# Optimization experiments

Hardware: AMD Instinct MI355X
Metric: run time of the kernel (lower is better)

The kernel has to match this reference:

```python
import jax, jax.numpy as jnp
import numpy as np

B, S, D = 2, 2048, 1024
H, DH = 16, 64
BS = 512            # block_size
MAX_LEN = 2048      # rope base = max_seq_length
NB = S // BS        # number of blocks (no padding: S % BS == 0)


def setup_inputs() -> dict:
    key = jax.random.key(0)
    ks = jax.random.split(key, 5)
    s = 1.0 / np.sqrt(D)
    x = jax.random.normal(ks[0], (B, S, D), jnp.float32)
    Wq = jax.random.normal(ks[1], (D, D), jnp.float32) * s
    Wk = jax.random.normal(ks[2], (D, D), jnp.float32) * s
    Wv = jax.random.normal(ks[3], (D, D), jnp.float32) * s
    Wo = jax.random.normal(ks[4], (D, D), jnp.float32) * s
    z = jnp.zeros((D,), jnp.float32)
    return {"x": x, "Wq": Wq, "bq": z, "Wk": Wk, "bk": z,
            "Wv": Wv, "bv": z, "Wo": Wo, "bo": z}


def _apply_rope(q, k):
    # inv_freq uses max_seq_length as the base (as in the source module)
    inv_freq = 1.0 / MAX_LEN ** (jnp.arange(0, DH, 2, dtype=jnp.float32) / DH)  # [DH/2]
    pos = jnp.arange(S, dtype=jnp.float32)
    freqs = jnp.outer(pos, inv_freq)                 # [S, DH/2]
    cos = jnp.cos(freqs)[None, :, None, :]           # [1,S,1,DH/2]
    sin = jnp.sin(freqs)[None, :, None, :]
    half = DH // 2
    q1, q2 = q[..., :half], q[..., half:]
    k1, k2 = k[..., :half], k[..., half:]
    q_rot = jnp.concatenate([q1 * cos - q2 * sin, q1 * sin + q2 * cos], axis=-1)
    k_rot = jnp.concatenate([k1 * cos - k2 * sin, k1 * sin + k2 * cos], axis=-1)
    return q_rot, k_rot


def _block_attn(qb, q_start, kb, vb, k_start):
    # qb,kb,vb: [B,H,BS,DH]; returns attended [B,H,BS,DH], lse [B,H,BS]
    scale = 1.0 / jnp.sqrt(DH)
    scores = jnp.einsum('bhqd,bhkd->bhqk', qb, kb) * scale
    q_pos = jnp.arange(BS) + q_start
    k_pos = jnp.arange(BS) + k_start
    mask = (q_pos[:, None] >= k_pos[None, :])[None, None]   # [1,1,BS,BS]
    scores = jnp.where(mask, scores, -1e9)
    mx = jnp.max(scores, axis=-1, keepdims=True)
    mx = jnp.where(jnp.isinf(mx), 0.0, mx)
    e = jnp.where(mask, jnp.exp(scores - mx), 0.0)
    se = jnp.sum(e, axis=-1, keepdims=True) + 1e-10
    attended = jnp.einsum('bhqk,bhkd->bhqd', e / se, vb)
    lse = (jnp.log(se) + mx)[..., 0]                        # [B,H,BS]
    return attended, lse


def _forward(x, Wq, bq, Wk, bk, Wv, bv, Wo, bo):
    q = (x @ Wq + bq).reshape(B, S, H, DH)
    k = (x @ Wk + bk).reshape(B, S, H, DH)
    v = (x @ Wv + bv).reshape(B, S, H, DH)
    q, k = _apply_rope(q, k)
    # split into blocks: [NB, B, H, BS, DH]
    def to_blocks(t):
        return t.reshape(B, NB, BS, H, DH).transpose(1, 0, 3, 2, 4)
    qb, kb, vb = to_blocks(q), to_blocks(k), to_blocks(v)
    starts = jnp.arange(NB) * BS
    inner = jax.vmap(_block_attn, in_axes=(None, None, 0, 0, 0))   # over k blocks
    outer = jax.vmap(inner, in_axes=(0, 0, None, None, None))      # over q blocks
    att, lse = outer(qb, starts, kb, vb, starts)
    # att: [NBq,NBk,B,H,BS,DH], lse: [NBq,NBk,B,H,BS]
    mlse = jnp.max(lse, axis=1, keepdims=True)
    w = jnp.exp(lse - mlse)
    w = w / (jnp.sum(w, axis=1, keepdims=True) + 1e-10)
    acc = jnp.sum(att * w[..., None], axis=1)                      # [NBq,B,H,BS,DH]
    out = acc.transpose(1, 0, 3, 2, 4).reshape(B, S, D)
    out = out @ Wo + bo
    return out


def reference(x, Wq, bq, Wk, bk, Wv, bv, Wo, bo):
    out = _forward(x, Wq, bq, Wk, bk, Wv, bv, Wo, bo)
    attention_weights = jnp.ones((B, H, S, S), jnp.float32)  # dummy, as in source
    return out, attention_weights
```

## Files before the change

kernel.cpp:

```cpp
#include <hip/hip_runtime.h>
#include <cstdint>
#include <cstddef>

#define DEVINL __device__ __forceinline__

typedef float   f32x4  __attribute__((ext_vector_type(4)));
typedef float   vf4    __attribute__((ext_vector_type(4)));
typedef __bf16  bf16x8 __attribute__((ext_vector_type(8)));
typedef uint32_t u32;
typedef unsigned short u16;
typedef uint32_t u32x4 __attribute__((ext_vector_type(4)));

constexpr int Bb = 2, Ss = 2048, Dd = 1024, Hh = 16;
constexpr int Mm = Bb * Ss;


DEVINL u16 f2bf(float f) {
  union { float f; u32 u; } a; a.f = f;
  u32 r = a.u + 0x7fffu + ((a.u >> 16) & 1u);
  return (u16)(r >> 16);
}

typedef const __attribute__((address_space(1))) void* gas_t;
typedef __attribute__((address_space(3))) void* las_t;
DEVINL void gld_lds16(const void* g, void* l) {
  __builtin_amdgcn_global_load_lds((gas_t)g, (las_t)l, 16, 0, 0);
}

__global__ void fill_ones(vf4* __restrict__ p, long long n4) {
  size_t i = (size_t)blockIdx.x * blockDim.x + threadIdx.x;
  size_t stride = (size_t)gridDim.x * blockDim.x;
  const vf4 one = {1.f, 1.f, 1.f, 1.f};
  for (; i < (size_t)n4; i += stride)
    __builtin_nontemporal_store(one, p + i);
}

__global__ void rope_table(float* __restrict__ cosT, float* __restrict__ sinT) {
  int idx = blockIdx.x * 256 + threadIdx.x;
  int s = idx >> 5, j = idx & 31;
  float freq = (float)s * exp2f(-11.0f * (float)j / 32.0f);
  cosT[idx] = cosf(freq);
  sinT[idx] = sinf(freq);
}

__global__ void cast_x(const float* __restrict__ x, u16* __restrict__ xb) {
  size_t i = ((size_t)blockIdx.x * 256 + threadIdx.x) * 4;
  vf4 v = *(const vf4*)(x + i);
  union { u16 u[4]; unsigned long long q; } o;
  o.u[0] = f2bf(v.x); o.u[1] = f2bf(v.y); o.u[2] = f2bf(v.z); o.u[3] = f2bf(v.w);
  *(unsigned long long*)(xb + i) = o.q;
}

__global__ void transpose_cast_W(const float* __restrict__ W0, const float* __restrict__ W1,
                                 const float* __restrict__ W2, const float* __restrict__ W3,
                                 u16* __restrict__ Wt) {
  __shared__ u16 tile[64][72];
  const int z = blockIdx.z;
  const float* W = (z == 0) ? W0 : (z == 1) ? W1 : (z == 2) ? W2 : W3;
  u16* Out = Wt + (size_t)z * (Dd * Dd);
  const int k0 = blockIdx.x * 64, n0 = blockIdx.y * 64;
  const int tid = threadIdx.x;
#pragma unroll
  for (int it = 0; it < 4; ++it) {
    int r = it * 16 + (tid >> 4);
    int c = (tid & 15) * 4;
    vf4 v = *(const vf4*)(W + (size_t)(k0 + r) * Dd + n0 + c);
    tile[r][c + 0] = f2bf(v.x); tile[r][c + 1] = f2bf(v.y);
    tile[r][c + 2] = f2bf(v.z); tile[r][c + 3] = f2bf(v.w);
  }
  __syncthreads();
#pragma unroll
  for (int it = 0; it < 2; ++it) {
    int c = it * 256 + tid;
    int n = c >> 3, ck = c & 7;
    union { u16 u[8]; u32x4 q; } o;
#pragma unroll
    for (int j = 0; j < 8; ++j) o.u[j] = tile[ck * 8 + j][n];
    *(u32x4*)(Out + (size_t)(n0 + n) * Dd + k0 + ck * 8) = o.q;
  }
}

DEVINL void gemm_mainloop(const u16* __restrict__ A, const u16* __restrict__ Bt,
                          int m0, int n0, char* lds, f32x4 (&acc)[4][4],
                          vf4* __restrict__ onesp, size_t obase) {
  const int tid = threadIdx.x, lane = tid & 63;
  const int w = tid >> 6, wr = w >> 1, wc = w & 1;
  const int l15 = lane & 15, l4 = lane >> 4;
  auto stage = [&](const u16* g, int row0, int k0, char* dst) {
#pragma unroll
    for (int h2 = 0; h2 < 2; ++h2) {
      int c = h2 * 256 + tid;
      const char* src = (const char*)g + (size_t)(row0 + (c >> 2)) * 2048 + k0 * 2 + (c & 3) * 16;
      gld_lds16(src, dst + c * 16);
    }
  };
  stage(A, m0, 0, lds);
  stage(Bt, n0, 0, lds + 16384);
  asm volatile("s_waitcnt vmcnt(0)");
  __syncthreads();
  const vf4 onev = {1.f, 1.f, 1.f, 1.f};
#pragma unroll 2
  for (int t = 0; t < 32; ++t) {
    const int cur = t & 1;
    char* As = lds + cur * 8192;
    char* Bs = lds + 16384 + cur * 8192;
    if (t < 31) {
      char* An = lds + (cur ^ 1) * 8192;
      char* Bn = lds + 16384 + (cur ^ 1) * 8192;
      stage(A, m0, (t + 1) * 32, An);
      stage(Bt, n0, (t + 1) * 32, Bn);
    }
    __builtin_nontemporal_store(onev, onesp + obase + (size_t)t * 256 + tid);
    bf16x8 af[4], bfr[4];
#pragma unroll
    for (int mt = 0; mt < 4; ++mt)
      af[mt] = *(const bf16x8*)(As + (wr * 64 + mt * 16 + l15) * 64 + l4 * 16);
#pragma unroll
    for (int nt = 0; nt < 4; ++nt)
      bfr[nt] = *(const bf16x8*)(Bs + (wc * 64 + nt * 16 + l15) * 64 + l4 * 16);
#pragma unroll
    for (int mt = 0; mt < 4; ++mt)
#pragma unroll
      for (int nt = 0; nt < 4; ++nt)
        acc[mt][nt] = __builtin_amdgcn_mfma_f32_16x16x32_bf16(af[mt], bfr[nt], acc[mt][nt], 0, 0, 0);
    asm volatile("s_waitcnt vmcnt(0)");
    __syncthreads();
  }
}

template <int EPI>
__global__ __launch_bounds__(256) void gemm128(
    const u16* __restrict__ A, const u16* __restrict__ W0,
    const float* __restrict__ b0, const float* __restrict__ b1, const float* __restrict__ b2,
    const float* __restrict__ cosT, const float* __restrict__ sinT,
    u16* __restrict__ Qo, u16* __restrict__ Ko, u16* __restrict__ Vo,
    float* __restrict__ outp, vf4* __restrict__ onesp) {
  __shared__ __align__(16) char lds[32768];
  const int tid = threadIdx.x, lane = tid & 63;
  const int w = tid >> 6, wr = w >> 1, wc = w & 1;
  const int l15 = lane & 15, l4 = lane >> 4;

  const int lin = blockIdx.y * 32 + blockIdx.x;
  const int xcd = lin & 7, ix = lin >> 3;
  constexpr int YPX = (EPI == 0) ? 3 : 1;
  const int ytile = xcd * YPX + (ix >> 5);
  const int m0 = (ix & 31) * 128;

  int mat, n0;
  const u16* Bt;
  if (EPI == 0) { mat = ytile >> 3; n0 = (ytile & 7) * 128; Bt = W0 + (size_t)mat * (Dd * Dd); }
  else          { mat = 0;          n0 = ytile * 128;       Bt = W0; }
  const size_t obase = (EPI == 0 ? 0 : (size_t)6291456) + (size_t)lin * 8192;

  f32x4 acc[4][4] = {};
  gemm_mainloop(A, Bt, m0, n0, lds, acc, onesp, obase);

  if (EPI == 0) {
    const float* bias = (mat == 0) ? b0 : ((mat == 1) ? b1 : b2);
    u16* Out = (mat == 0) ? Qo : ((mat == 1) ? Ko : Vo);
    const bool dorope = (mat < 2);
#pragma unroll
    for (int mt = 0; mt < 4; ++mt) {
#pragma unroll
      for (int i = 0; i < 4; ++i) {
        int m = m0 + wr * 64 + mt * 16 + l4 * 4 + i;
        int bidx = m >> 11, s = m & 2047;
        float cv0 = 0.f, sv0 = 0.f, cv1 = 0.f, sv1 = 0.f;
        if (dorope) {
          cv0 = cosT[s * 32 + l15];      sv0 = sinT[s * 32 + l15];
          cv1 = cosT[s * 32 + 16 + l15]; sv1 = sinT[s * 32 + 16 + l15];
        }
#pragma unroll
        for (int nt = 0; nt < 4; ++nt) {
          int n = n0 + wc * 64 + nt * 16 + l15;
          float v = acc[mt][nt][i] + bias[n];
          float ov;
          if (dorope) {
            int np = n0 + wc * 64 + (nt ^ 2) * 16 + l15;
            float vp = acc[mt][nt ^ 2][i] + bias[np];
            float cc = (nt & 1) ? cv1 : cv0, sn = (nt & 1) ? sv1 : sv0;
            ov = (nt < 2) ? (v * cc - vp * sn)
                          : (vp * sn + v * cc);
          } else ov = v;
          int hh = n >> 6, dh = n & 63;
          Out[(((size_t)bidx * Hh + hh) * Ss + s) * 64 + dh] = f2bf(ov);
        }
      }
    }
  } else {
#pragma unroll
    for (int mt = 0; mt < 4; ++mt)
#pragma unroll
      for (int i = 0; i < 4; ++i) {
        int m = m0 + wr * 64 + mt * 16 + l4 * 4 + i;
#pragma unroll
        for (int nt = 0; nt < 4; ++nt) {
          int n = n0 + wc * 64 + nt * 16 + l15;
          outp[(size_t)m * Dd + n] = acc[mt][nt][i] + b0[n];
        }
      }
  }
}

__global__ void transpose_v(const u16* __restrict__ Vg, u16* __restrict__ Vtg) {
  __shared__ u16 tile[64][72];
  const int s0 = blockIdx.x * 64, bh = blockIdx.y;
  const int tid = threadIdx.x;
  const u16* Vb = Vg + (size_t)bh * Ss * 64;
  u16* Vtb = Vtg + (size_t)bh * 64 * Ss;
#pragma unroll
  for (int h2 = 0; h2 < 2; ++h2) {
    int c = h2 * 256 + tid;
    int r = c >> 3, ck = c & 7;
    u32x4 v = *(const u32x4*)(Vb + (size_t)(s0 + r) * 64 + ck * 8);
    const u16* t8 = (const u16*)&v;
#pragma unroll
    for (int j = 0; j < 8; ++j) tile[r][ck * 8 + j] = t8[j];
  }
  __syncthreads();
#pragma unroll
  for (int h2 = 0; h2 < 2; ++h2) {
    int c = h2 * 256 + tid;
    int dh = c >> 3, ck = c & 7;
    union { u16 u[8]; u32x4 q; } o;
#pragma unroll
    for (int j = 0; j < 8; ++j) o.u[j] = tile[ck * 8 + j][dh];
    *(u32x4*)(Vtb + (size_t)dh * Ss + s0 + ck * 8) = o.q;
  }
}

__global__ __launch_bounds__(256) void attn_kernel(
    const u16* __restrict__ Qg, const u16* __restrict__ Kg,
    const u16* __restrict__ Vtg, u16* __restrict__ Og) {
  __shared__ __align__(16) char lds[49152];

  const int tid = threadIdx.x, lane = tid & 63, w = tid >> 6;
  const int l15 = lane & 15, l4 = lane >> 4;

  const int bid = blockIdx.x;
  const int bh = bid & 31;
  const int qt_raw = (bid >> 5) & 7;
  const int qtile = (bid >> 8) ? qt_raw : (15 - qt_raw);
  const int q0 = qtile * 128;
  const int qw = q0 + w * 32;
  const int ntiles = 2 * qtile + 2;
  const int tdiag = qw >> 6;

  const u16*  Qb  = Qg + (size_t)bh * Ss * 64;
  const char* Kb  = (const char*)(Kg + (size_t)bh * Ss * 64);
  const char* Vtb = (const char*)(Vtg + (size_t)bh * 64 * Ss);

  bf16x8 aq[2][2];
#pragma unroll
  for (int mt = 0; mt < 2; ++mt)
#pragma unroll
    for (int kt = 0; kt < 2; ++kt)
      aq[mt][kt] = *(const bf16x8*)(Qb + (size_t)(qw + mt * 16 + l15) * 64 + kt * 32 + l4 * 8);

  f32x4 accO[2][4] = {};
  float mrow[2][4], lrow[2][4];
#pragma unroll
  for (int mt = 0; mt < 2; ++mt)
#pragma unroll
    for (int i = 0; i < 4; ++i) { mrow[mt][i] = -1e30f; lrow[mt][i] = 0.f; }

  char* pw = lds + 32768 + w * 4096;

  auto stageKV = [&](int t, char* bK, char* bV) {
    const int kv0 = t * 64;
#pragma unroll
    for (int h2 = 0; h2 < 2; ++h2) {
      int c = h2 * 256 + tid;
      int r = c >> 3, ck = c & 7;
      gld_lds16(Kb + (size_t)(kv0 + r) * 128 + ((ck ^ (r & 7)) * 16), bK + c * 16);
      gld_lds16(Vtb + (size_t)r * (Ss * 2) + (size_t)kv0 * 2 + ((ck ^ (r & 7)) * 16), bV + c * 16);
    }
  };

  stageKV(0, lds, lds + 8192);
  asm volatile("s_waitcnt vmcnt(0)");
  __syncthreads();

  for (int t = 0; t < ntiles; ++t) {
    const int cur = t & 1;
    char* curb = lds + cur * 16384;
    char* nxtb = lds + (cur ^ 1) * 16384;
    if (t + 1 < ntiles) stageKV(t + 1, nxtb, nxtb + 8192);
    if (t <= tdiag) {
      const int kv0 = t * 64;
      char* ldsK = curb;
      char* ldsV = curb + 8192;

      f32x4 sf[2][4] = {};
#pragma unroll
      for (int kt = 0; kt < 2; ++kt) {
        bf16x8 bk[4];
#pragma unroll
        for (int nt = 0; nt < 4; ++nt) {
          int row = nt * 16 + l15;
          int ch = (kt * 4 + l4) ^ (row & 7);
          bk[nt] = *(const bf16x8*)(ldsK + row * 128 + ch * 16);
        }
#pragma unroll
        for (int mt = 0; mt < 2; ++mt)
#pragma unroll
          for (int nt = 0; nt < 4; ++nt)
            sf[mt][nt] = __builtin_amdgcn_mfma_f32_16x16x32_bf16(aq[mt][kt], bk[nt], sf[mt][nt], 0, 0, 0);
      }

      const bool diag = (t == tdiag);
#pragma unroll
      for (int mt = 0; mt < 2; ++mt) {
#pragma unroll
        for (int i = 0; i < 4; ++i) {
          int row = qw + mt * 16 + l4 * 4 + i;
          float sv[4];
          float mx = -1e30f;
#pragma unroll
          for (int nt = 0; nt < 4; ++nt) {
            float xv = sf[mt][nt][i] * 0.125f;
            if (diag && (kv0 + nt * 16 + l15) > row) xv = -1e30f;
            sv[nt] = xv; mx = fmaxf(mx, xv);
          }
          mx = fmaxf(mx, __shfl_xor(mx, 1));
          mx = fmaxf(mx, __shfl_xor(mx, 2));
          mx = fmaxf(mx, __shfl_xor(mx, 4));
          mx = fmaxf(mx, __shfl_xor(mx, 8));
          float mnew = fmaxf(mrow[mt][i], mx);
          float rescale = __expf(mrow[mt][i] - mnew);
          float rs = 0.f;
          int rl = mt * 16 + l4 * 4 + i;
#pragma unroll
          for (int nt = 0; nt < 4; ++nt) {
            float p = __expf(sv[nt] - mnew);
            rs += p;
            int key = nt * 16 + l15;
            int boff = rl * 128 + (((key >> 3) ^ (rl & 7)) << 4) + (key & 7) * 2;
            *(u16*)(pw + boff) = f2bf(p);
          }
          rs += __shfl_xor(rs, 1); rs += __shfl_xor(rs, 2);
          rs += __shfl_xor(rs, 4); rs += __shfl_xor(rs, 8);
          lrow[mt][i] = lrow[mt][i] * rescale + rs;
          mrow[mt][i] = mnew;
#pragma unroll
          for (int nt = 0; nt < 4; ++nt) accO[mt][nt][i] *= rescale;
        }
      }

#pragma unroll
      for (int ks = 0; ks < 2; ++ks) {
        bf16x8 ap[2], bv[4];
#pragma unroll
        for (int mt = 0; mt < 2; ++mt) {
          int row = mt * 16 + l15;
          int ch = (ks * 4 + l4) ^ (row & 7);
          ap[mt] = *(const bf16x8*)(pw + row * 128 + ch * 16);
        }
#pragma unroll
        for (int nt = 0; nt < 4; ++nt) {
          int row = nt * 16 + l15;
          int ch = (ks * 4 + l4) ^ (row & 7);
          bv[nt] = *(const bf16x8*)(ldsV + row * 128 + ch * 16);
        }
#pragma unroll
        for (int mt = 0; mt < 2; ++mt)
#pragma unroll
          for (int nt = 0; nt < 4; ++nt)
            accO[mt][nt] = __builtin_amdgcn_mfma_f32_16x16x32_bf16(ap[mt], bv[nt], accO[mt][nt], 0, 0, 0);
      }
    }
    asm volatile("s_waitcnt vmcnt(0)");
    __syncthreads();
  }

  const int b = bh >> 4, h = bh & 15;
#pragma unroll
  for (int mt = 0; mt < 2; ++mt)
#pragma unroll
    for (int i = 0; i < 4; ++i) {
      int s = qw + mt * 16 + l4 * 4 + i;
      float inv = 1.0f / (lrow[mt][i] + 1e-10f);
      size_t rowbase = ((size_t)b * Ss + s) * Dd + h * 64;
#pragma unroll
      for (int nt = 0; nt < 4; ++nt)
        Og[rowbase + nt * 16 + l15] = f2bf(accO[mt][nt][i] * inv);
    }
}

extern "C" void kernel_launch(void* const* d_in, const int* in_sizes, int n_in,
                              void* d_out, int out_size, void* d_ws, size_t ws_size,
                              hipStream_t stream) {
  const float* x  = (const float*)d_in[0];
  const float* Wq = (const float*)d_in[1];
  const float* bq = (const float*)d_in[2];
  const float* Wk = (const float*)d_in[3];
  const float* bk = (const float*)d_in[4];
  const float* Wv = (const float*)d_in[5];
  const float* bv = (const float*)d_in[6];
  const float* Wo = (const float*)d_in[7];
  const float* bo = (const float*)d_in[8];
  float* out = (float*)d_out;

  char* ws = (char*)d_ws;
  u16*   xb   = (u16*)(ws);
  u16*   Wt   = (u16*)(ws + ((size_t)8 << 20));
  float* cosT = (float*)(ws + ((size_t)16 << 20));
  float* sinT = (float*)(ws + ((size_t)16 << 20) + ((size_t)256 << 10));
  u16*   Qg   = (u16*)(ws + ((size_t)17 << 20));
  u16*   Kg   = (u16*)(ws + ((size_t)25 << 20));
  u16*   Vg   = (u16*)(ws + ((size_t)33 << 20));
  u16*   Vtg  = (u16*)(ws + ((size_t)41 << 20));
  u16*   Og   = (u16*)(ws + ((size_t)49 << 20));

  size_t ones_off = (size_t)Mm * Dd;
  vf4* onesp = (vf4*)(out + ones_off);
  const long long n4_total = ((long long)out_size - (long long)ones_off) / 4;
  const long long n4_side  = 8388608;
  fill_ones<<<2048, 256, 0, stream>>>(onesp + n4_side, n4_total - n4_side);

  rope_table<<<256, 256, 0, stream>>>(cosT, sinT);
  cast_x<<<(Mm * Dd) / 1024, 256, 0, stream>>>(x, xb);
  transpose_cast_W<<<dim3(16, 16, 4), 256, 0, stream>>>(Wq, Wk, Wv, Wo, Wt);

  gemm128<0><<<dim3(32, 24), 256, 0, stream>>>(xb, Wt, bq, bk, bv, cosT, sinT,
                                               Qg, Kg, Vg, nullptr, onesp);
  transpose_v<<<dim3(32, 32), 256, 0, stream>>>(Vg, Vtg);
  attn_kernel<<<512, 256, 0, stream>>>(Qg, Kg, Vtg, Og);
  gemm128<1><<<dim3(32, 8), 256, 0, stream>>>(Og, Wt + (size_t)3 * Dd * Dd,
                                              bo, nullptr, nullptr, nullptr, nullptr,
                                              nullptr, nullptr, nullptr, out, onesp);
}
```

Baseline: 732.8 us.

## Drop attention LDS staging, read K/V directly per wave, shift ones-fill into GEMMs

```diff
diff --git a/kernel.cpp b/kernel.cpp
--- a/kernel.cpp
+++ b/kernel.cpp
@@ -96,7 +96,6 @@
   };
   stage(A, m0, 0, lds);
   stage(Bt, n0, 0, lds + 16384);
-  asm volatile("s_waitcnt vmcnt(0)");
   __syncthreads();
   const vf4 onev = {1.f, 1.f, 1.f, 1.f};
 #pragma unroll 2
@@ -110,7 +109,8 @@
       stage(A, m0, (t + 1) * 32, An);
       stage(Bt, n0, (t + 1) * 32, Bn);
     }
-    __builtin_nontemporal_store(onev, onesp + obase + (size_t)t * 256 + tid);
+    __builtin_nontemporal_store(onev, onesp + obase + (size_t)t * 512 + tid);
+    __builtin_nontemporal_store(onev, onesp + obase + (size_t)t * 512 + 256 + tid);
     bf16x8 af[4], bfr[4];
 #pragma unroll
     for (int mt = 0; mt < 4; ++mt)
@@ -123,7 +123,6 @@
 #pragma unroll
       for (int nt = 0; nt < 4; ++nt)
         acc[mt][nt] = __builtin_amdgcn_mfma_f32_16x16x32_bf16(af[mt], bfr[nt], acc[mt][nt], 0, 0, 0);
-    asm volatile("s_waitcnt vmcnt(0)");
     __syncthreads();
   }
 }
@@ -150,7 +149,7 @@
   const u16* Bt;
   if (EPI == 0) { mat = ytile >> 3; n0 = (ytile & 7) * 128; Bt = W0 + (size_t)mat * (Dd * Dd); }
   else          { mat = 0;          n0 = ytile * 128;       Bt = W0; }
-  const size_t obase = (EPI == 0 ? 0 : (size_t)6291456) + (size_t)lin * 8192;
+  const size_t obase = (EPI == 0 ? 0 : (size_t)12582912) + (size_t)lin * 16384;
 
   f32x4 acc[4][4] = {};
   gemm_mainloop(A, Bt, m0, n0, lds, acc, onesp, obase);
@@ -232,7 +231,7 @@
 __global__ __launch_bounds__(256) void attn_kernel(
     const u16* __restrict__ Qg, const u16* __restrict__ Kg,
     const u16* __restrict__ Vtg, u16* __restrict__ Og) {
-  __shared__ __align__(16) char lds[49152];
+  __shared__ __align__(16) char lds[16384];
 
   const int tid = threadIdx.x, lane = tid & 63, w = tid >> 6;
   const int l15 = lane & 15, l4 = lane >> 4;
@@ -241,9 +240,7 @@
   const int bh = bid & 31;
   const int qt_raw = (bid >> 5) & 7;
   const int qtile = (bid >> 8) ? qt_raw : (15 - qt_raw);
-  const int q0 = qtile * 128;
-  const int qw = q0 + w * 32;
-  const int ntiles = 2 * qtile + 2;
+  const int qw = qtile * 128 + w * 32;
   const int tdiag = qw >> 6;
 
   const u16*  Qb  = Qg + (size_t)bh * Ss * 64;
@@ -264,113 +261,86 @@
 #pragma unroll
     for (int i = 0; i < 4; ++i) { mrow[mt][i] = -1e30f; lrow[mt][i] = 0.f; }
 
-  char* pw = lds + 32768 + w * 4096;
-
-  auto stageKV = [&](int t, char* bK, char* bV) {
+  char* pw = lds + w * 4096;
+
+  for (int t = 0; t <= tdiag; ++t) {
     const int kv0 = t * 64;
-#pragma unroll
-    for (int h2 = 0; h2 < 2; ++h2) {
-      int c = h2 * 256 + tid;
-      int r = c >> 3, ck = c & 7;
-      gld_lds16(Kb + (size_t)(kv0 + r) * 128 + ((ck ^ (r & 7)) * 16), bK + c * 16);
-      gld_lds16(Vtb + (size_t)r * (Ss * 2) + (size_t)kv0 * 2 + ((ck ^ (r & 7)) * 16), bV + c * 16);
-    }
-  };
-
-  stageKV(0, lds, lds + 8192);
-  asm volatile("s_waitcnt vmcnt(0)");
-  __syncthreads();
-
-  for (int t = 0; t < ntiles; ++t) {
-    const int cur = t & 1;
-    char* curb = lds + cur * 16384;
-    char* nxtb = lds + (cur ^ 1) * 16384;
-    if (t + 1 < ntiles) stageKV(t + 1, nxtb, nxtb + 8192);
-    if (t <= tdiag) {
-      const int kv0 = t * 64;
-      char* ldsK = curb;
-      char* ldsV = curb + 8192;
-
-      f32x4 sf[2][4] = {};
-#pragma unroll
-      for (int kt = 0; kt < 2; ++kt) {
-        bf16x8 bk[4];
+
+    f32x4 sf[2][4] = {};
+#pragma unroll
+    for (int kt = 0; kt < 2; ++kt) {
+      bf16x8 bk[4];
+#pragma unroll
+      for (int nt = 0; nt < 4; ++nt)
+        bk[nt] = *(const bf16x8*)(Kb + (size_t)(kv0 + nt * 16 + l15) * 128 + kt * 64 + l4 * 16);
+      __builtin_amdgcn_s_setprio(1);
+#pragma unroll
+      for (int mt = 0; mt < 2; ++mt)
+#pragma unroll
+        for (int nt = 0; nt < 4; ++nt)
+          sf[mt][nt] = __builtin_amdgcn_mfma_f32_16x16x32_bf16(aq[mt][kt], bk[nt], sf[mt][nt], 0, 0, 0);
+      __builtin_amdgcn_s_setprio(0);
+    }
+
+    const bool diag = (t == tdiag);
+#pragma unroll
+    for (int mt = 0; mt < 2; ++mt) {
+#pragma unroll
+      for (int i = 0; i < 4; ++i) {
+        int row = qw + mt * 16 + l4 * 4 + i;
+        float sv[4];
+        float mx = -1e30f;
 #pragma unroll
         for (int nt = 0; nt < 4; ++nt) {
-          int row = nt * 16 + l15;
-          int ch = (kt * 4 + l4) ^ (row & 7);
-          bk[nt] = *(const bf16x8*)(ldsK + row * 128 + ch * 16);
+          float xv = sf[mt][nt][i] * 0.125f;
+          if (diag && (kv0 + nt * 16 + l15) > row) xv = -1e30f;
+          sv[nt] = xv; mx = fmaxf(mx, xv);
         }
-#pragma unroll
-        for (int mt = 0; mt < 2; ++mt)
-#pragma unroll
-          for (int nt = 0; nt < 4; ++nt)
-            sf[mt][nt] = __builtin_amdgcn_mfma_f32_16x16x32_bf16(aq[mt][kt], bk[nt], sf[mt][nt], 0, 0, 0);
+        mx = fmaxf(mx, __shfl_xor(mx, 1));
+        mx = fmaxf(mx, __shfl_xor(mx, 2));
+        mx = fmaxf(mx, __shfl_xor(mx, 4));
+        mx = fmaxf(mx, __shfl_xor(mx, 8));
+        float mnew = fmaxf(mrow[mt][i], mx);
+        float rescale = __expf(mrow[mt][i] - mnew);
+        float rs = 0.f;
+        int rl = mt * 16 + l4 * 4 + i;
+#pragma unroll
+        for (int nt = 0; nt < 4; ++nt) {
+          float p = __expf(sv[nt] - mnew);
+          rs += p;
+          int key = nt * 16 + l15;
+          int boff = rl * 128 + (((key >> 3) ^ (rl & 7)) << 4) + (key & 7) * 2;
+          *(u16*)(pw + boff) = f2bf(p);
+        }
+        rs += __shfl_xor(rs, 1); rs += __shfl_xor(rs, 2);
+        rs += __shfl_xor(rs, 4); rs += __shfl_xor(rs, 8);
+        lrow[mt][i] = lrow[mt][i] * rescale + rs;
+        mrow[mt][i] = mnew;
+#pragma unroll
+        for (int nt = 0; nt < 4; ++nt) accO[mt][nt][i] *= rescale;
       }
-
-      const bool diag = (t == tdiag);
+    }
+
+#pragma unroll
+    for (int ks = 0; ks < 2; ++ks) {
+      bf16x8 ap[2], bv[4];
 #pragma unroll
       for (int mt = 0; mt < 2; ++mt) {
-#pragma unroll
-        for (int i = 0; i < 4; ++i) {
-          int row = qw + mt * 16 + l4 * 4 + i;
-          float sv[4];
-          float mx = -1e30f;
-#pragma unroll
-          for (int nt = 0; nt < 4; ++nt) {
-            float xv = sf[mt][nt][i] * 0.125f;
-            if (diag && (kv0 + nt * 16 + l15) > row) xv = -1e30f;
-            sv[nt] = xv; mx = fmaxf(mx, xv);
-          }
-          mx = fmaxf(mx, __shfl_xor(mx, 1));
-          mx = fmaxf(mx, __shfl_xor(mx, 2));
-          mx = fmaxf(mx, __shfl_xor(mx, 4));
-          mx = fmaxf(mx, __shfl_xor(mx, 8));
-          float mnew = fmaxf(mrow[mt][i], mx);
-          float rescale = __expf(mrow[mt][i] - mnew);
-          float rs = 0.f;
-          int rl = mt * 16 + l4 * 4 + i;
-#pragma unroll
-          for (int nt = 0; nt < 4; ++nt) {
-            float p = __expf(sv[nt] - mnew);
-            rs += p;
-            int key = nt * 16 + l15;
-            int boff = rl * 128 + (((key >> 3) ^ (rl & 7)) << 4) + (key & 7) * 2;
-            *(u16*)(pw + boff) = f2bf(p);
-          }
-          rs += __shfl_xor(rs, 1); rs += __shfl_xor(rs, 2);
-          rs += __shfl_xor(rs, 4); rs += __shfl_xor(rs, 8);
-          lrow[mt][i] = lrow[mt][i] * rescale + rs;
-          mrow[mt][i] = mnew;
-#pragma unroll
-          for (int nt = 0; nt < 4; ++nt) accO[mt][nt][i] *= rescale;
-        }
+        int row = mt * 16 + l15;
+        int ch = (ks * 4 + l4) ^ (row & 7);
+        ap[mt] = *(const bf16x8*)(pw + row * 128 + ch * 16);
       }
-
-#pragma unroll
-      for (int ks = 0; ks < 2; ++ks) {
-        bf16x8 ap[2], bv[4];
-#pragma unroll
-        for (int mt = 0; mt < 2; ++mt) {
-          int row = mt * 16 + l15;
-          int ch = (ks * 4 + l4) ^ (row & 7);
-          ap[mt] = *(const bf16x8*)(pw + row * 128 + ch * 16);
-        }
-#pragma unroll
-        for (int nt = 0; nt < 4; ++nt) {
-          int row = nt * 16 + l15;
-          int ch = (ks * 4 + l4) ^ (row & 7);
-          bv[nt] = *(const bf16x8*)(ldsV + row * 128 + ch * 16);
-        }
-#pragma unroll
-        for (int mt = 0; mt < 2; ++mt)
-#pragma unroll
-          for (int nt = 0; nt < 4; ++nt)
-            accO[mt][nt] = __builtin_amdgcn_mfma_f32_16x16x32_bf16(ap[mt], bv[nt], accO[mt][nt], 0, 0, 0);
-      }
-    }
-    asm volatile("s_waitcnt vmcnt(0)");
-    __syncthreads();
+#pragma unroll
+      for (int nt = 0; nt < 4; ++nt)
+        bv[nt] = *(const bf16x8*)(Vtb + (size_t)(nt * 16 + l15) * (Ss * 2) + (size_t)kv0 * 2 + ks * 64 + l4 * 16);
+      __builtin_amdgcn_s_setprio(1);
+#pragma unroll
+      for (int mt = 0; mt < 2; ++mt)
+#pragma unroll
+        for (int nt = 0; nt < 4; ++nt)
+          accO[mt][nt] = __builtin_amdgcn_mfma_f32_16x16x32_bf16(ap[mt], bv[nt], accO[mt][nt], 0, 0, 0);
+      __builtin_amdgcn_s_setprio(0);
+    }
   }
 
   const int b = bh >> 4, h = bh & 15;
@@ -415,7 +385,7 @@
   size_t ones_off = (size_t)Mm * Dd;
   vf4* onesp = (vf4*)(out + ones_off);
   const long long n4_total = ((long long)out_size - (long long)ones_off) / 4;
-  const long long n4_side  = 8388608;
+  const long long n4_side  = 16777216;
   fill_ones<<<2048, 256, 0, stream>>>(onesp + n4_side, n4_total - n4_side);
 
   rope_table<<<256, 256, 0, stream>>>(cosT, sinT);
```

Result: no change. 731.9 us (-0.1%).
